# Performance work log

Measured on AMD Instinct MI355X. Metric: run time of the kernel, lower is better.

The kernel has to match this reference:

```python
import jax, jax.numpy as jnp
import numpy as np

B, N, DIN, D, E, STEP = 4, 1024, 256, 256, 5, 5


def setup_inputs() -> dict:
    key = jax.random.key(0)
    ks = jax.random.split(key, 14)
    s = 0.02  # weight init scale
    inp = {
        "node_features": jax.random.normal(ks[0], (B, N, DIN), dtype=jnp.float32),
        # dense per-edge-type adjacency; scaled so messages stay in a sane range
        "adj_matrices": jax.random.uniform(ks[1], (B, E, N, N), dtype=jnp.float32) * (2.0 / N),
        "fc_in_w": jax.random.normal(ks[2], (D, DIN), dtype=jnp.float32) * s,
        "fc_in_b": jnp.zeros((D,), dtype=jnp.float32),
        "edge_w": jax.random.normal(ks[3], (E, D, D), dtype=jnp.float32) * s,
        "edge_b": jax.random.normal(ks[4], (E, D), dtype=jnp.float32) * s,
        "gru_w_ih": jax.random.normal(ks[5], (3 * D, D), dtype=jnp.float32) * s,
        "gru_w_hh": jax.random.normal(ks[6], (3 * D, D), dtype=jnp.float32) * s,
        "gru_b_ih": jnp.zeros((3 * D,), dtype=jnp.float32),
        "gru_b_hh": jnp.zeros((3 * D,), dtype=jnp.float32),
        "conv1_w": jax.random.normal(ks[7], (D, D), dtype=jnp.float32) * s,
        "conv1_b": jnp.zeros((D,), dtype=jnp.float32),
        "conv2_w": jax.random.normal(ks[8], (D, D), dtype=jnp.float32) * s,
        "conv2_b": jnp.zeros((D,), dtype=jnp.float32),
    }
    return inp


def _gru_cell(x, h, w_ih, w_hh, b_ih, b_hh):
    # torch GRUCell: gates ordered [r, z, n]
    gi = x @ w_ih.T + b_ih  # [B*N, 3D]
    gh = h @ w_hh.T + b_hh
    ir, iz, inn = jnp.split(gi, 3, axis=-1)
    hr, hz, hn = jnp.split(gh, 3, axis=-1)
    r = jax.nn.sigmoid(ir + hr)
    z = jax.nn.sigmoid(iz + hz)
    n = jnp.tanh(inn + r * hn)
    return (1.0 - z) * n + z * h


def reference(node_features, adj_matrices, fc_in_w, fc_in_b, edge_w, edge_b,
              gru_w_ih, gru_w_hh, gru_b_ih, gru_b_hh,
              conv1_w, conv1_b, conv2_w, conv2_b):
    h = node_features @ fc_in_w.T + fc_in_b  # [B, N, D]
    sum_edge_b = jnp.sum(edge_b, axis=0)  # accumulated biases over edge types
    for _ in range(STEP):
        # messages per edge type: adj_e @ h  -> [B, E, N, D]
        msgs = jnp.einsum('benm,bmd->bend', adj_matrices, h)
        # per-edge-type linear (y = x @ W_e.T) then accumulate over edge types
        acc = jnp.einsum('bend,ekd->bnk', msgs, edge_w) + sum_edge_b  # [B, N, D]
        h = _gru_cell(acc, h, gru_w_ih, gru_w_hh, gru_b_ih, gru_b_hh)
    node_states = h  # [B, N, D]
    # conv1d with kernel_size=1 over node axis == per-node linear on channels
    attn_weights = jax.nn.sigmoid(node_states @ conv1_w.T + conv1_b)  # [B, N, D]
    feats = jnp.tanh(node_states @ conv2_w.T + conv2_b)  # [B, N, D]
    graph_embedding = jnp.sum(attn_weights * feats, axis=1)  # sum over nodes -> [B, D]
    attn_map = jnp.mean(attn_weights, axis=2)  # mean over channels -> [B, N]
    return (graph_embedding, node_states, attn_map)
```

## Files before the change

kernel.cpp:

```cpp
#include <hip/hip_runtime.h>
#include <hip/hip_bf16.h>
#include <cstdint>


typedef __attribute__((ext_vector_type(8))) short bf16x8;
typedef __attribute__((ext_vector_type(4))) float f32x4;

__device__ __forceinline__ float bf2f(__hip_bfloat16 x) { return __bfloat162float(x); }
__device__ __forceinline__ __hip_bfloat16 f2bf(float x) { return __float2bfloat16(x); }
__device__ __forceinline__ short f2bs(float x) {
  __hip_bfloat16 h = __float2bfloat16(x);
  return *reinterpret_cast<short*>(&h);
}
__device__ __forceinline__ float s2f(short x) {
  __hip_bfloat16 h = *reinterpret_cast<__hip_bfloat16*>(&x);
  return __bfloat162float(h);
}

__device__ __forceinline__ bf16x8 ld8_ext(const void* base, long off, bool f32) {
  if (f32) {
    const float* p = (const float*)base + off;
    bf16x8 r;
#pragma unroll
    for (int i = 0; i < 8; ++i) r[i] = f2bs(p[i]);
    return r;
  }
  return *(const bf16x8*)((const __hip_bfloat16*)base + off);
}

__device__ __forceinline__ bf16x8 ld8_sum5(const __hip_bfloat16* part, int row, int k) {
  const long base = (long)row * 256 + (long)(row >> 10) * 1048576 + k;
  float s[8] = {0.f, 0.f, 0.f, 0.f, 0.f, 0.f, 0.f, 0.f};
#pragma unroll
  for (int e = 0; e < 5; ++e) {
    bf16x8 v = *(const bf16x8*)(part + base + e * 262144);
#pragma unroll
// ... 56 lines not shown
}

__global__ void wcvt_all(const void* fcw, const void* edw, const void* wih,
                         const void* whh, const void* c1w, const void* c2w,
                         const int* __restrict__ flag, __hip_bfloat16* __restrict__ dst) {
  const bool f32 = (*flag != 0);
  const int i = blockIdx.x * 256 + threadIdx.x;
  const void* src; int off;
  if      (i < 65536)  { src = fcw; off = i; }
  else if (i < 393216) { src = edw; off = i - 65536; }
  else if (i < 589824) { src = wih; off = i - 393216; }
  else if (i < 786432) { src = whh; off = i - 589824; }
  else if (i < 851968) { src = c1w; off = i - 786432; }
  else                 { src = c2w; off = i - 851968; }
  dst[i] = f32 ? f2bf(((const float*)src)[off])
               : ((const __hip_bfloat16*)src)[off];
}

__global__ void adj_cvt(const void* __restrict__ src, const int* __restrict__ flag,
                        __hip_bfloat16* __restrict__ dst) {
  const bool f32 = (*flag != 0);
  const long i = ((long)blockIdx.x * 256 + threadIdx.x) * 8;
  bf16x8 r;
  if (f32) {
    const float* p = (const float*)src + i;
#pragma unroll
    for (int j = 0; j < 8; ++j) r[j] = f2bs(p[j]);
  } else {
    r = *(const bf16x8*)((const __hip_bfloat16*)src + i);
  }
  *(bf16x8*)(dst + i) = r;
}

template<bool HAS_BIAS, bool DUAL>
__global__ __launch_bounds__(256)
void gemm_bt128(const __hip_bfloat16* __restrict__ A, const __hip_bfloat16* __restrict__ Bt,
                const float* __restrict__ bias, __hip_bfloat16* __restrict__ C,
                const __hip_bfloat16* __restrict__ A2, const __hip_bfloat16* __restrict__ Bt2,
                const float* __restrict__ bias2, __hip_bfloat16* __restrict__ C2,
                int K, int lda, int ldb, int ldc,
                long aBatch, int zdivA, int zmodA,
                long bBatch, int zdivB, int zmodB,
                long cBatch, int zdivC, int zSplit)
{
  __shared__ __align__(16) __hip_bfloat16 sA[128 * 64];
  __shared__ __align__(16) __hip_bfloat16 sB[64 * 64];
  const int t = threadIdx.x;
  const int w = t >> 6;
  const int l = t & 63;
  const int m0 = blockIdx.x * 128;
  const int n0 = blockIdx.y * 64;
  int z = blockIdx.z;

  const __hip_bfloat16* Au = A; const __hip_bfloat16* Btu = Bt;
  const float* biasu = bias; __hip_bfloat16* Cu = C;
  if (DUAL && z >= zSplit) { Au = A2; Btu = Bt2; biasu = bias2; Cu = C2; z -= zSplit; }

  const __hip_bfloat16* Ab = Au + (long)((z / zdivA) % zmodA) * aBatch;
  const __hip_bfloat16* Bb = Btu + (long)((z / zdivB) % zmodB) * bBatch;

  int sra[4], sca[4];
#pragma unroll
  for (int i = 0; i < 4; ++i) {
    const int p = t + 256 * i;
    sra[i] = p >> 3;
    sca[i] = (p & 7) ^ (sra[i] & 7);
  }
  const int p0 = t, p1 = t + 256;
  const int sr0 = p0 >> 3, sc0 = (p0 & 7) ^ (sr0 & 7);
  const int sr1 = p1 >> 3, sc1 = (p1 & 7) ^ (sr1 & 7);

  f32x4 acc[2][4];
#pragma unroll
  for (int i = 0; i < 2; ++i)
#pragma unroll
    for (int j = 0; j < 4; ++j) acc[i][j] = (f32x4){0.f, 0.f, 0.f, 0.f};

  const int r15 = l & 15;
  const int quad = l >> 4;

  for (int k0 = 0; k0 < K; k0 += 64) {
    bf16x8 av[4];
#pragma unroll
    for (int i = 0; i < 4; ++i)
      av[i] = *(const bf16x8*)(Ab + (long)(m0 + sra[i]) * lda + (k0 + sca[i] * 8));
    bf16x8 b0 = *(const bf16x8*)(Bb + (long)(n0 + sr0) * ldb + (k0 + sc0 * 8));
    bf16x8 b1 = *(const bf16x8*)(Bb + (long)(n0 + sr1) * ldb + (k0 + sc1 * 8));
    __syncthreads();
#pragma unroll
    for (int i = 0; i < 4; ++i) *(bf16x8*)(sA + (t + 256 * i) * 8) = av[i];
    *(bf16x8*)(sB + p0 * 8) = b0;
    *(bf16x8*)(sB + p1 * 8) = b1;
    __syncthreads();
#pragma unroll
    for (int ks = 0; ks < 2; ++ks) {
      const int cg = ks * 4 + quad;
      bf16x8 aF[2], bF[4];
#pragma unroll
      for (int mi = 0; mi < 2; ++mi) {
        const int row = mi * 64 + w * 16 + r15;
        aF[mi] = *(const bf16x8*)(sA + row * 64 + ((cg ^ (row & 7)) * 8));
      }
#pragma unroll
      for (int ni = 0; ni < 4; ++ni) {
        const int nrow = ni * 16 + r15;
        bF[ni] = *(const bf16x8*)(sB + nrow * 64 + ((cg ^ (nrow & 7)) * 8));
      }
#pragma unroll
      for (int mi = 0; mi < 2; ++mi)
#pragma unroll
        for (int ni = 0; ni < 4; ++ni)
          acc[mi][ni] = __builtin_amdgcn_mfma_f32_16x16x32_bf16(
              aF[mi], bF[ni], acc[mi][ni], 0, 0, 0);
    }
  }

  const long cOff = (long)(z / zdivC) * cBatch;
#pragma unroll
  for (int mi = 0; mi < 2; ++mi) {
#pragma unroll
    for (int ni = 0; ni < 4; ++ni) {
      const int n = n0 + ni * 16 + r15;
      float bv = 0.f;
      if (HAS_BIAS) bv = biasu[n];
#pragma unroll
      for (int r = 0; r < 4; ++r) {
        const int m = m0 + mi * 64 + w * 16 + quad * 4 + r;
        Cu[cOff + (long)m * ldc + n] = f2bf(acc[mi][ni][r] + bv);
      }
    }
  }
}

__global__ __launch_bounds__(256)
void part_gh(const __hip_bfloat16* __restrict__ adjb,
             const __hip_bfloat16* __restrict__ heT,
             __hip_bfloat16* __restrict__ part,
             const __hip_bfloat16* __restrict__ hbf,
             const __hip_bfloat16* __restrict__ whh,
             const float* __restrict__ bhh,
             __hip_bfloat16* __restrict__ gh)
{
  __shared__ __align__(16) __hip_bfloat16 sA[128 * 64];
  __shared__ __align__(16) __hip_bfloat16 sB[64 * 64];
  const int t = threadIdx.x;
  const int w = t >> 6;
  const int l = t & 63;
  const int bid = blockIdx.x;

  const __hip_bfloat16* Ab; const __hip_bfloat16* Bb;
  __hip_bfloat16* Cu; const float* biasu = nullptr;
  int K, lda, ldb, ldc, m0, n0;
  bool has_bias;
  if (bid < 640) {
    const int z = bid >> 5, rem = bid & 31;
    m0 = (rem & 7) * 128; n0 = (rem >> 3) * 64;
    Ab = adjb + (long)z * 1048576; lda = 1024; K = 1024;
    Bb = heT + (long)z * 262144;  ldb = 1024;
    Cu = part + (long)z * 262144; ldc = 256;
    has_bias = false;
  } else {
    const int idx = bid - 640;
    m0 = (idx & 31) * 128; n0 = (idx >> 5) * 64;
    Ab = hbf; lda = 256; K = 256;
    Bb = whh; ldb = 256;
    Cu = gh;  ldc = 768;
    biasu = bhh; has_bias = true;
  }

  int sra[4], sca[4];
#pragma unroll
  for (int i = 0; i < 4; ++i) {
    const int p = t + 256 * i;
    sra[i] = p >> 3;
    sca[i] = (p & 7) ^ (sra[i] & 7);
  }
  const int p0 = t, p1 = t + 256;
  const int sr0 = p0 >> 3, sc0 = (p0 & 7) ^ (sr0 & 7);
  const int sr1 = p1 >> 3, sc1 = (p1 & 7) ^ (sr1 & 7);

  f32x4 acc[2][4];
#pragma unroll
  for (int i = 0; i < 2; ++i)
#pragma unroll
    for (int j = 0; j < 4; ++j) acc[i][j] = (f32x4){0.f, 0.f, 0.f, 0.f};

  const int r15 = l & 15;
  const int quad = l >> 4;

  for (int k0 = 0; k0 < K; k0 += 64) {
    bf16x8 av[4];
#pragma unroll
    for (int i = 0; i < 4; ++i)
      av[i] = *(const bf16x8*)(Ab + (long)(m0 + sra[i]) * lda + (k0 + sca[i] * 8));
    bf16x8 b0 = *(const bf16x8*)(Bb + (long)(n0 + sr0) * ldb + (k0 + sc0 * 8));
    bf16x8 b1 = *(const bf16x8*)(Bb + (long)(n0 + sr1) * ldb + (k0 + sc1 * 8));
    __syncthreads();
#pragma unroll
    for (int i = 0; i < 4; ++i) *(bf16x8*)(sA + (t + 256 * i) * 8) = av[i];
    *(bf16x8*)(sB + p0 * 8) = b0;
    *(bf16x8*)(sB + p1 * 8) = b1;
    __syncthreads();
#pragma unroll
    for (int ks = 0; ks < 2; ++ks) {
      const int cg = ks * 4 + quad;
      bf16x8 aF[2], bF[4];
#pragma unroll
      for (int mi = 0; mi < 2; ++mi) {
        const int row = mi * 64 + w * 16 + r15;
        aF[mi] = *(const bf16x8*)(sA + row * 64 + ((cg ^ (row & 7)) * 8));
      }
#pragma unroll
      for (int ni = 0; ni < 4; ++ni) {
        const int nrow = ni * 16 + r15;
        bF[ni] = *(const bf16x8*)(sB + nrow * 64 + ((cg ^ (nrow & 7)) * 8));
      }
#pragma unroll
      for (int mi = 0; mi < 2; ++mi)
#pragma unroll
        for (int ni = 0; ni < 4; ++ni)
          acc[mi][ni] = __builtin_amdgcn_mfma_f32_16x16x32_bf16(
              aF[mi], bF[ni], acc[mi][ni], 0, 0, 0);
    }
  }

#pragma unroll
  for (int mi = 0; mi < 2; ++mi) {
#pragma unroll
    for (int ni = 0; ni < 4; ++ni) {
      const int n = n0 + ni * 16 + r15;
      const float bv = has_bias ? biasu[n] : 0.f;
#pragma unroll
      for (int r = 0; r < 4; ++r) {
        const int m = m0 + mi * 64 + w * 16 + quad * 4 + r;
        Cu[(long)m * ldc + n] = f2bf(acc[mi][ni][r] + bv);
      }
    }
  }
}

__global__ __launch_bounds__(256)
void gi_gate(const __hip_bfloat16* __restrict__ part,
             const __hip_bfloat16* __restrict__ wih,
             const float* __restrict__ biasgi,
             const __hip_bfloat16* __restrict__ gh,
             __hip_bfloat16* __restrict__ hbf,
             void* __restrict__ ns_out, const int* __restrict__ flag)
{
  __shared__ __align__(16) __hip_bfloat16 sA[64 * 64];
  __shared__ __align__(16) __hip_bfloat16 sB0[64 * 64];
  __shared__ __align__(16) __hip_bfloat16 sB1[64 * 64];
  __shared__ __align__(16) __hip_bfloat16 sB2[64 * 64];
  const int t = threadIdx.x;
  const int w = t >> 6;
  const int l = t & 63;
  const int m0 = (blockIdx.x & 63) * 64;
  const int n0 = (blockIdx.x >> 6) * 64;

  const int p0 = t, p1 = t + 256;
  const int sr0 = p0 >> 3, sc0 = (p0 & 7) ^ (sr0 & 7);
  const int sr1 = p1 >> 3, sc1 = (p1 & 7) ^ (sr1 & 7);

  f32x4 acc[3][4];
#pragma unroll
  for (int g = 0; g < 3; ++g)
#pragma unroll
    for (int j = 0; j < 4; ++j) acc[g][j] = (f32x4){0.f, 0.f, 0.f, 0.f};

  const int mrow = w * 16 + (l & 15);
  const int r15 = l & 15;
  const int quad = l >> 4;

  for (int k0 = 0; k0 < 256; k0 += 64) {
    bf16x8 a0 = ld8_sum5(part, m0 + sr0, k0 + sc0 * 8);
    bf16x8 a1 = ld8_sum5(part, m0 + sr1, k0 + sc1 * 8);
    bf16x8 bg[3][2];
#pragma unroll
    for (int g = 0; g < 3; ++g) {
      bg[g][0] = *(const bf16x8*)(wih + (long)(g * 256 + n0 + sr0) * 256 + (k0 + sc0 * 8));
      bg[g][1] = *(const bf16x8*)(wih + (long)(g * 256 + n0 + sr1) * 256 + (k0 + sc1 * 8));
    }
    __syncthreads();
    *(bf16x8*)(sA + p0 * 8) = a0;
    *(bf16x8*)(sA + p1 * 8) = a1;
    *(bf16x8*)(sB0 + p0 * 8) = bg[0][0]; *(bf16x8*)(sB0 + p1 * 8) = bg[0][1];
    *(bf16x8*)(sB1 + p0 * 8) = bg[1][0]; *(bf16x8*)(sB1 + p1 * 8) = bg[1][1];
    *(bf16x8*)(sB2 + p0 * 8) = bg[2][0]; *(bf16x8*)(sB2 + p1 * 8) = bg[2][1];
    __syncthreads();
#pragma unroll
    for (int ks = 0; ks < 2; ++ks) {
      const int cg = ks * 4 + quad;
      bf16x8 af = *(const bf16x8*)(sA + mrow * 64 + ((cg ^ (mrow & 7)) * 8));
#pragma unroll
      for (int t4 = 0; t4 < 4; ++t4) {
        const int nrow = t4 * 16 + r15;
        const int so = nrow * 64 + ((cg ^ (nrow & 7)) * 8);
        bf16x8 b0f = *(const bf16x8*)(sB0 + so);
        bf16x8 b1f = *(const bf16x8*)(sB1 + so);
        bf16x8 b2f = *(const bf16x8*)(sB2 + so);
        acc[0][t4] = __builtin_amdgcn_mfma_f32_16x16x32_bf16(af, b0f, acc[0][t4], 0, 0, 0);
        acc[1][t4] = __builtin_amdgcn_mfma_f32_16x16x32_bf16(af, b1f, acc[1][t4], 0, 0, 0);
        acc[2][t4] = __builtin_amdgcn_mfma_f32_16x16x32_bf16(af, b2f, acc[2][t4], 0, 0, 0);
      }
    }
  }

  const bool f32out = ns_out && (*flag != 0);
#pragma unroll
  for (int t4 = 0; t4 < 4; ++t4) {
    const int n = n0 + t4 * 16 + r15;
    const float bgr = biasgi[n];
    const float bgz = biasgi[256 + n];
    const float bgn = biasgi[512 + n];
#pragma unroll
    for (int r = 0; r < 4; ++r) {
      const int m = m0 + w * 16 + quad * 4 + r;
      const long gb = (long)m * 768;
      const float ir = acc[0][t4][r] + bgr;
      const float iz = acc[1][t4][r] + bgz;
      const float inn = acc[2][t4][r] + bgn;
      const float hr = bf2f(gh[gb + n]);
      const float hz = bf2f(gh[gb + 256 + n]);
      const float hn = bf2f(gh[gb + 512 + n]);
      const long hidx = (long)m * 256 + n;
      const float h = bf2f(hbf[hidx]);
      const float rr = 1.f / (1.f + __expf(-(ir + hr)));
      const float zz = 1.f / (1.f + __expf(-(iz + hz)));
      const float nn = tanhf(inn + rr * hn);
      const float hnew = (1.f - zz) * nn + zz * h;
      const __hip_bfloat16 hb = f2bf(hnew);
      hbf[hidx] = hb;
      if (ns_out) {
        if (f32out) ((float*)ns_out)[1024 + hidx] = hnew;
        else        ((__hip_bfloat16*)ns_out)[1024 + hidx] = hb;
      }
    }
  }
}

template<int OUT_MODE, bool HAS_BIAS, int A_MODE, bool DUAL>
__global__ __launch_bounds__(256)
void gemm_bt(const void* __restrict__ A, const __hip_bfloat16* __restrict__ Bt,
             const float* __restrict__ bias, void* __restrict__ Cp,
             const void* __restrict__ A2, const __hip_bfloat16* __restrict__ Bt2,
             const float* __restrict__ bias2, void* __restrict__ Cp2,
             const int* __restrict__ flag,
             int Kg, int ngrp, int lda, int ldb, int ldc,
             long aBatch, int zdivA, int zmodA,
             long bBatch, int zdivB, int zmodB,
             long cBatch, int zdivC, long aGrp, long bGrp, int zSplit)
{
  __shared__ __align__(16) __hip_bfloat16 sA[64 * 64];
  __shared__ __align__(16) __hip_bfloat16 sB[64 * 64];
  const bool af32 = (A_MODE == 1) ? (*flag != 0) : false;
  const int t = threadIdx.x;
  const int w = t >> 6;
  const int l = t & 63;
  const int m0 = blockIdx.x * 64;
  const int n0 = blockIdx.y * 64;
  int z = blockIdx.z;

  const void* Au = A; const __hip_bfloat16* Btu = Bt;
  const float* biasu = bias; void* Cpu = Cp;
  bool second = false;
  if (DUAL && z >= zSplit) {
    Au = A2; Btu = Bt2; biasu = bias2; Cpu = Cp2; z -= zSplit; second = true;
  }

  const long aOff = (long)((z / zdivA) % zmodA) * aBatch;
  const __hip_bfloat16* Bb = Btu + (long)((z / zdivB) % zmodB) * bBatch;
// ... 81 lines not shown
  bf16x8 vhz = *(const bf16x8*)(gh + gb + 256);
  bf16x8 vhn = *(const bf16x8*)(gh + gb + 512);
  const long hidx = (long)m * 256 + k;
  bf16x8 vh = *(const bf16x8*)(hbf + hidx);
  bf16x8 out;
  float hf[8];
#pragma unroll
  for (int j = 0; j < 8; ++j) {
    const float r = 1.f / (1.f + __expf(-(s2f(vir[j]) + s2f(vhr[j]))));
    const float zz = 1.f / (1.f + __expf(-(s2f(viz[j]) + s2f(vhz[j]))));
    const float nn = tanhf(s2f(vin[j]) + r * s2f(vhn[j]));
    hf[j] = (1.f - zz) * nn + zz * s2f(vh[j]);
    out[j] = f2bs(hf[j]);
  }
  *(bf16x8*)(hbf + hidx) = out;
  if (ns_out) {
    if (*flag) {
      float* o = (float*)ns_out + 1024 + hidx;
#pragma unroll
      for (int j = 0; j < 8; ++j) o[j] = hf[j];
    } else {
      *(bf16x8*)((__hip_bfloat16*)ns_out + 1024 + hidx) = out;
    }
  }
}

__global__ __launch_bounds__(256)
void conv_fused(const __hip_bfloat16* __restrict__ hbf,
                const __hip_bfloat16* __restrict__ c1w,
                const __hip_bfloat16* __restrict__ c2w,
                const float* __restrict__ pool,
                float* __restrict__ geg, float* __restrict__ am32)
{
  __shared__ __align__(16) __hip_bfloat16 sA[64 * 64];
  __shared__ __align__(16) __hip_bfloat16 sB1[64 * 64];
  __shared__ __align__(16) __hip_bfloat16 sB2[64 * 64];
  __shared__ float sge[64];
  __shared__ float sam[64];
  const int t = threadIdx.x, w = t >> 6, l = t & 63;
  const int m0 = blockIdx.x * 64, n0 = blockIdx.y * 64;
  if (t < 64) { sge[t] = 0.f; sam[t] = 0.f; }
  const int p0 = t, p1 = t + 256;
  const int sr0 = p0 >> 3, sc0 = (p0 & 7) ^ (sr0 & 7);
  const int sr1 = p1 >> 3, sc1 = (p1 & 7) ^ (sr1 & 7);
  f32x4 a1[4], a2[4];
#pragma unroll
  for (int i = 0; i < 4; ++i) { a1[i] = (f32x4){0,0,0,0}; a2[i] = (f32x4){0,0,0,0}; }
  const int mrow = w * 16 + (l & 15);
  const int quad = l >> 4;
  for (int k0 = 0; k0 < 256; k0 += 64) {
    bf16x8 va0 = *(const bf16x8*)(hbf + (long)(m0 + sr0) * 256 + (k0 + sc0 * 8));
    bf16x8 va1 = *(const bf16x8*)(hbf + (long)(m0 + sr1) * 256 + (k0 + sc1 * 8));
    bf16x8 vb0 = *(const bf16x8*)(c1w + (long)(n0 + sr0) * 256 + (k0 + sc0 * 8));
    bf16x8 vb1 = *(const bf16x8*)(c1w + (long)(n0 + sr1) * 256 + (k0 + sc1 * 8));
    bf16x8 vc0 = *(const bf16x8*)(c2w + (long)(n0 + sr0) * 256 + (k0 + sc0 * 8));
    bf16x8 vc1 = *(const bf16x8*)(c2w + (long)(n0 + sr1) * 256 + (k0 + sc1 * 8));
    __syncthreads();
    *(bf16x8*)(sA + p0 * 8) = va0;  *(bf16x8*)(sA + p1 * 8) = va1;
    *(bf16x8*)(sB1 + p0 * 8) = vb0; *(bf16x8*)(sB1 + p1 * 8) = vb1;
    *(bf16x8*)(sB2 + p0 * 8) = vc0; *(bf16x8*)(sB2 + p1 * 8) = vc1;
    __syncthreads();
#pragma unroll
    for (int ks = 0; ks < 2; ++ks) {
      const int cg = ks * 4 + quad;
      bf16x8 af = *(const bf16x8*)(sA + mrow * 64 + ((cg ^ (mrow & 7)) * 8));
#pragma unroll
      for (int t4 = 0; t4 < 4; ++t4) {
        const int nrow = t4 * 16 + (l & 15);
        bf16x8 b1f = *(const bf16x8*)(sB1 + nrow * 64 + ((cg ^ (nrow & 7)) * 8));
        bf16x8 b2f = *(const bf16x8*)(sB2 + nrow * 64 + ((cg ^ (nrow & 7)) * 8));
        a1[t4] = __builtin_amdgcn_mfma_f32_16x16x32_bf16(af, b1f, a1[t4], 0, 0, 0);
        a2[t4] = __builtin_amdgcn_mfma_f32_16x16x32_bf16(af, b2f, a2[t4], 0, 0, 0);
      }
    }
  }
  float asum[4] = {0.f, 0.f, 0.f, 0.f};
#pragma unroll
  for (int t4 = 0; t4 < 4; ++t4) {
    const int n = n0 + t4 * 16 + (l & 15);
    const float bb1 = pool[1792 + n], bb2 = pool[2048 + n];
    float g = 0.f;
#pragma unroll
    for (int r = 0; r < 4; ++r) {
      const float av = 1.f / (1.f + __expf(-(a1[t4][r] + bb1)));
      const float fv = tanhf(a2[t4][r] + bb2);
      g += av * fv;
      asum[r] += av;
    }
    atomicAdd(&sge[t4 * 16 + (l & 15)], g);
  }
#pragma unroll
  for (int r = 0; r < 4; ++r) atomicAdd(&sam[w * 16 + quad * 4 + r], asum[r]);
  __syncthreads();
  if (t < 64) atomicAdd(&geg[(m0 >> 10) * 256 + n0 + t], sge[t]);
  else if (t < 128) atomicAdd(&am32[m0 + (t - 64)], sam[t - 64]);
}

__global__ void finish_out(const float* __restrict__ ge, const float* __restrict__ am32,
                           void* __restrict__ dout, const int* __restrict__ flag)
{
  const int t = blockIdx.x * 256 + threadIdx.x;
  const bool f32 = (*flag != 0);
  if (t < 1024) {
    if (f32) ((float*)dout)[t] = ge[t];
    else     ((__hip_bfloat16*)dout)[t] = f2bf(ge[t]);
  } else {
    const float v = am32[t - 1024] * (1.f / 256.f);
    if (f32) ((float*)dout)[1049600 + t - 1024] = v;
    else     ((__hip_bfloat16*)dout)[1049600 + t - 1024] = f2bf(v);
  }
}

extern "C" void kernel_launch(void* const* d_in, const int* in_sizes, int n_in,
                              void* d_out, int out_size, void* d_ws, size_t ws_size,
                              hipStream_t stream) {
  (void)in_sizes; (void)n_in; (void)out_size;
  const void* node_f = d_in[0];
  const void* adj    = d_in[1];
  const void* fc_w   = d_in[2];
  const void* fc_b   = d_in[3];
  const void* edge_w = d_in[4];
  const void* edge_b = d_in[5];
  const void* w_ih   = d_in[6];
  const void* w_hh   = d_in[7];
  const void* b_ih   = d_in[8];
  const void* b_hh   = d_in[9];
  const void* c1w    = d_in[10];
  const void* c1b    = d_in[11];
  const void* c2w    = d_in[12];
  const void* c2b    = d_in[13];

  char* ws = (char*)d_ws;
  const size_t MB = (size_t)1 << 20;
  int*            flag = (int*)(ws);
  float*          bp   = (float*)(ws + 256);
  float*          ge   = (float*)(ws + 14336);
  float*          am32 = (float*)(ws + 18432);
  __hip_bfloat16* wbf  = (__hip_bfloat16*)(ws + 34816);
  __hip_bfloat16* hbf  = (__hip_bfloat16*)(ws + 1869824);
  char*           S    = ws + 3966976;
  __hip_bfloat16* heT  = (__hip_bfloat16*)(S);
  __hip_bfloat16* part = (__hip_bfloat16*)(S + 10 * MB);
  __hip_bfloat16* gi   = (__hip_bfloat16*)(S + 20 * MB);
  __hip_bfloat16* gh   = (__hip_bfloat16*)(S + 26 * MB);
  __hip_bfloat16* adjb = (__hip_bfloat16*)(ws + 40 * MB);

  const bool has_split = ws_size >= 38 * MB;
  const bool has_adjb  = ws_size >= 81 * MB;

  detect_dtype<<<1, 256, 0, stream>>>((const uint32_t*)adj, flag);
  prep_pool<<<1, 256, 0, stream>>>(fc_b, b_ih, b_hh, c1b, c2b, edge_b, flag, bp, ge, am32);
  wcvt_all<<<3584, 256, 0, stream>>>(fc_w, edge_w, w_ih, w_hh, c1w, c2w, flag, wbf);
  bias_gi_k<<<3, 256, 0, stream>>>(bp, wbf + 393216, bp + 2560);
  if (has_adjb) adj_cvt<<<10240, 256, 0, stream>>>(adj, flag, adjb);

  gemm_bt<0, true, 1, false><<<dim3(64, 4, 1), 256, 0, stream>>>(
      node_f, wbf + 0, bp + 0, hbf, nullptr, nullptr, nullptr, nullptr, flag,
      256, 1, 256, 256, 256, 0, 1, 1, 0, 1, 1, 0, 1, 0, 0, 0);

  for (int s = 0; s < 5; ++s) {
    if (has_adjb) {
      gemm_bt128<false, false><<<dim3(2, 16, 20), 256, 0, stream>>>(
          wbf + 65536, hbf, nullptr, heT, nullptr, nullptr, nullptr, nullptr,
          256, 256, 256, 1024,
          65536, 1, 5,
          262144, 5, 4,
          262144, 1, 0);
      part_gh<<<1024, 256, 0, stream>>>(adjb, heT, part,
                                        hbf, wbf + 589824, bp + 1024, gh);
      gi_gate<<<256, 256, 0, stream>>>(part, wbf + 393216, bp + 2560, gh, hbf,
                                       (s == 4) ? d_out : nullptr, flag);
    } else if (has_split) {
      gemm_bt<0, false, 0, false><<<dim3(4, 16, 20), 256, 0, stream>>>(
          wbf + 65536, hbf, nullptr, heT, nullptr, nullptr, nullptr, nullptr, flag,
          256, 1, 256, 256, 1024,
          65536, 1, 5, 262144, 5, 4,
          262144, 1, 0, 0, 0);
      gemm_bt<0, false, 1, false><<<dim3(16, 4, 20), 256, 0, stream>>>(
          adj, heT, nullptr, part, nullptr, nullptr, nullptr, nullptr, flag,
          1024, 1, 1024, 1024, 256,
          1048576, 1, 20, 262144, 1, 20,
          262144, 1, 0, 0, 0);
      gemm_bt<0, true, 2, true><<<dim3(64, 12, 2), 256, 0, stream>>>(
          part, wbf + 393216, bp + 2560, gi,
          hbf,  wbf + 589824, bp + 1024, gh, flag,
          256, 1, 256, 256, 768, 0, 1, 1, 0, 1, 1, 0, 1, 0, 0, 1);
      gru_gate8<<<512, 256, 0, stream>>>(gi, gh, hbf,
                                         (s == 4) ? d_out : nullptr, flag);
    } else {
      gemm_bt<0, false, 0, false><<<dim3(4, 16, 20), 256, 0, stream>>>(
          wbf + 65536, hbf, nullptr, heT, nullptr, nullptr, nullptr, nullptr, flag,
          256, 1, 256, 256, 1024,
          65536, 1, 5, 262144, 5, 4,
          262144, 1, 0, 0, 0);
      gemm_bt<0, true, 1, false><<<dim3(16, 4, 4), 256, 0, stream>>>(
          adj, heT, bp + 2304, part, nullptr, nullptr, nullptr, nullptr, flag,
          1024, 5, 1024, 1024, 256,
          (long)5 * 1048576, 1, 4, (long)5 * 262144, 1, 4,
          262144, 1, 1048576, 262144, 0);
      gemm_bt<0, true, 0, true><<<dim3(64, 12, 2), 256, 0, stream>>>(
          part, wbf + 393216, bp + 256, gi,
          hbf,  wbf + 589824, bp + 1024, gh, flag,
          256, 1, 256, 256, 768, 0, 1, 1, 0, 1, 1, 0, 1, 0, 0, 1);
      gru_gate8<<<512, 256, 0, stream>>>(gi, gh, hbf,
                                         (s == 4) ? d_out : nullptr, flag);
    }
  }

  conv_fused<<<dim3(64, 4), 256, 0, stream>>>(hbf, wbf + 786432, wbf + 851968,
                                              bp, ge, am32);
  finish_out<<<20, 256, 0, stream>>>(ge, am32, d_out, flag);
}
```

Baseline: 432.8 us.

## Fuse GGNN steps into one persistent cooperative kernel with grid syncs

```diff
diff --git a/kernel.cpp b/kernel.cpp
--- a/kernel.cpp
+++ b/kernel.cpp
@@ -1,7 +1,10 @@
 #include <hip/hip_runtime.h>
 #include <hip/hip_bf16.h>
+#include <hip/hip_cooperative_groups.h>
 #include <cstdint>
 
+
+namespace cg = cooperative_groups;
 
 typedef __attribute__((ext_vector_type(8))) short bf16x8;
 typedef __attribute__((ext_vector_type(4))) float f32x4;
@@ -124,33 +127,16 @@
   *(bf16x8*)(dst + i) = r;
 }
 
-template<bool HAS_BIAS, bool DUAL>
-__global__ __launch_bounds__(256)
-void gemm_bt128(const __hip_bfloat16* __restrict__ A, const __hip_bfloat16* __restrict__ Bt,
-                const float* __restrict__ bias, __hip_bfloat16* __restrict__ C,
-                const __hip_bfloat16* __restrict__ A2, const __hip_bfloat16* __restrict__ Bt2,
-                const float* __restrict__ bias2, __hip_bfloat16* __restrict__ C2,
-                int K, int lda, int ldb, int ldc,
-                long aBatch, int zdivA, int zmodA,
-                long bBatch, int zdivB, int zmodB,
-                long cBatch, int zdivC, int zSplit)
-{
-  __shared__ __align__(16) __hip_bfloat16 sA[128 * 64];
-  __shared__ __align__(16) __hip_bfloat16 sB[64 * 64];
-  const int t = threadIdx.x;
-  const int w = t >> 6;
-  const int l = t & 63;
-  const int m0 = blockIdx.x * 128;
-  const int n0 = blockIdx.y * 64;
-  int z = blockIdx.z;
-
-  const __hip_bfloat16* Au = A; const __hip_bfloat16* Btu = Bt;
-  const float* biasu = bias; __hip_bfloat16* Cu = C;
-  if (DUAL && z >= zSplit) { Au = A2; Btu = Bt2; biasu = bias2; Cu = C2; z -= zSplit; }
-
-  const __hip_bfloat16* Ab = Au + (long)((z / zdivA) % zmodA) * aBatch;
-  const __hip_bfloat16* Bb = Btu + (long)((z / zdivB) % zmodB) * bBatch;
-
+
+__device__ __forceinline__ void tile128(char* smem, int t,
+    const void* Abase, int lda, bool af32,
+    const __hip_bfloat16* Bb, int ldb,
+    const float* bias, __hip_bfloat16* C, int ldc,
+    int K, int m0, int n0)
+{
+  __hip_bfloat16* sA = (__hip_bfloat16*)smem;
+  __hip_bfloat16* sB = (__hip_bfloat16*)(smem + 16384);
+  const int w = t >> 6, l = t & 63;
   int sra[4], sca[4];
 #pragma unroll
   for (int i = 0; i < 4; ++i) {
@@ -175,7 +161,7 @@
     bf16x8 av[4];
 #pragma unroll
     for (int i = 0; i < 4; ++i)
-      av[i] = *(const bf16x8*)(Ab + (long)(m0 + sra[i]) * lda + (k0 + sca[i] * 8));
+      av[i] = ld8_ext(Abase, (long)(m0 + sra[i]) * lda + (k0 + sca[i] * 8), af32);
     bf16x8 b0 = *(const bf16x8*)(Bb + (long)(n0 + sr0) * ldb + (k0 + sc0 * 8));
     bf16x8 b1 = *(const bf16x8*)(Bb + (long)(n0 + sr1) * ldb + (k0 + sc1 * 8));
     __syncthreads();
@@ -207,152 +193,36 @@
     }
   }
 
-  const long cOff = (long)(z / zdivC) * cBatch;
+  const bool hasb = (bias != nullptr);
 #pragma unroll
   for (int mi = 0; mi < 2; ++mi) {
 #pragma unroll
     for (int ni = 0; ni < 4; ++ni) {
       const int n = n0 + ni * 16 + r15;
-      float bv = 0.f;
-      if (HAS_BIAS) bv = biasu[n];
+      const float bv = hasb ? bias[n] : 0.f;
 #pragma unroll
       for (int r = 0; r < 4; ++r) {
         const int m = m0 + mi * 64 + w * 16 + quad * 4 + r;
-        Cu[cOff + (long)m * ldc + n] = f2bf(acc[mi][ni][r] + bv);
+        C[(long)m * ldc + n] = f2bf(acc[mi][ni][r] + bv);
       }
     }
   }
 }
 
-__global__ __launch_bounds__(256)
-void part_gh(const __hip_bfloat16* __restrict__ adjb,
-             const __hip_bfloat16* __restrict__ heT,
-             __hip_bfloat16* __restrict__ part,
-             const __hip_bfloat16* __restrict__ hbf,
-             const __hip_bfloat16* __restrict__ whh,
-             const float* __restrict__ bhh,
-             __hip_bfloat16* __restrict__ gh)
-{
-  __shared__ __align__(16) __hip_bfloat16 sA[128 * 64];
-  __shared__ __align__(16) __hip_bfloat16 sB[64 * 64];
-  const int t = threadIdx.x;
-  const int w = t >> 6;
-  const int l = t & 63;
-  const int bid = blockIdx.x;
-
-  const __hip_bfloat16* Ab; const __hip_bfloat16* Bb;
-  __hip_bfloat16* Cu; const float* biasu = nullptr;
-  int K, lda, ldb, ldc, m0, n0;
-  bool has_bias;
-  if (bid < 640) {
-    const int z = bid >> 5, rem = bid & 31;
-    m0 = (rem & 7) * 128; n0 = (rem >> 3) * 64;
-    Ab = adjb + (long)z * 1048576; lda = 1024; K = 1024;
-    Bb = heT + (long)z * 262144;  ldb = 1024;
-    Cu = part + (long)z * 262144; ldc = 256;
-    has_bias = false;
-  } else {
-    const int idx = bid - 640;
-    m0 = (idx & 31) * 128; n0 = (idx >> 5) * 64;
-    Ab = hbf; lda = 256; K = 256;
-    Bb = whh; ldb = 256;
-    Cu = gh;  ldc = 768;
-    biasu = bhh; has_bias = true;
-  }
-
-  int sra[4], sca[4];
-#pragma unroll
-  for (int i = 0; i < 4; ++i) {
-    const int p = t + 256 * i;
-    sra[i] = p >> 3;
-    sca[i] = (p & 7) ^ (sra[i] & 7);
-  }
+__device__ __forceinline__ void gi_tile(char* smem, int t,
+    const __hip_bfloat16* ms, const __hip_bfloat16* wih,
+    const float* biasgi, const __hip_bfloat16* gh,
+    __hip_bfloat16* hbf, void* ns_out, bool f32flag, int m0, int n0)
+{
+  __hip_bfloat16* sA  = (__hip_bfloat16*)smem;
+  __hip_bfloat16* sB0 = (__hip_bfloat16*)(smem + 8192);
+  __hip_bfloat16* sB1 = (__hip_bfloat16*)(smem + 16384);
+  __hip_bfloat16* sB2 = (__hip_bfloat16*)(smem + 24576);
+  const int w = t >> 6, l = t & 63;
   const int p0 = t, p1 = t + 256;
   const int sr0 = p0 >> 3, sc0 = (p0 & 7) ^ (sr0 & 7);
   const int sr1 = p1 >> 3, sc1 = (p1 & 7) ^ (sr1 & 7);
 
-  f32x4 acc[2][4];
-#pragma unroll
-  for (int i = 0; i < 2; ++i)
-#pragma unroll
-    for (int j = 0; j < 4; ++j) acc[i][j] = (f32x4){0.f, 0.f, 0.f, 0.f};
-
-  const int r15 = l & 15;
-  const int quad = l >> 4;
-
-  for (int k0 = 0; k0 < K; k0 += 64) {
-    bf16x8 av[4];
-#pragma unroll
-    for (int i = 0; i < 4; ++i)
-      av[i] = *(const bf16x8*)(Ab + (long)(m0 + sra[i]) * lda + (k0 + sca[i] * 8));
-    bf16x8 b0 = *(const bf16x8*)(Bb + (long)(n0 + sr0) * ldb + (k0 + sc0 * 8));
-    bf16x8 b1 = *(const bf16x8*)(Bb + (long)(n0 + sr1) * ldb + (k0 + sc1 * 8));
-    __syncthreads();
-#pragma unroll
-    for (int i = 0; i < 4; ++i) *(bf16x8*)(sA + (t + 256 * i) * 8) = av[i];
-    *(bf16x8*)(sB + p0 * 8) = b0;
-    *(bf16x8*)(sB + p1 * 8) = b1;
-    __syncthreads();
-#pragma unroll
-    for (int ks = 0; ks < 2; ++ks) {
-      const int cg = ks * 4 + quad;
-      bf16x8 aF[2], bF[4];
-#pragma unroll
-      for (int mi = 0; mi < 2; ++mi) {
-        const int row = mi * 64 + w * 16 + r15;
-        aF[mi] = *(const bf16x8*)(sA + row * 64 + ((cg ^ (row & 7)) * 8));
-      }
-#pragma unroll
-      for (int ni = 0; ni < 4; ++ni) {
-        const int nrow = ni * 16 + r15;
-        bF[ni] = *(const bf16x8*)(sB + nrow * 64 + ((cg ^ (nrow & 7)) * 8));
-      }
-#pragma unroll
-      for (int mi = 0; mi < 2; ++mi)
-#pragma unroll
-        for (int ni = 0; ni < 4; ++ni)
-          acc[mi][ni] = __builtin_amdgcn_mfma_f32_16x16x32_bf16(
-              aF[mi], bF[ni], acc[mi][ni], 0, 0, 0);
-    }
-  }
-
-#pragma unroll
-  for (int mi = 0; mi < 2; ++mi) {
-#pragma unroll
-    for (int ni = 0; ni < 4; ++ni) {
-      const int n = n0 + ni * 16 + r15;
-      const float bv = has_bias ? biasu[n] : 0.f;
-#pragma unroll
-      for (int r = 0; r < 4; ++r) {
-        const int m = m0 + mi * 64 + w * 16 + quad * 4 + r;
-        Cu[(long)m * ldc + n] = f2bf(acc[mi][ni][r] + bv);
-      }
-    }
-  }
-}
-
-__global__ __launch_bounds__(256)
-void gi_gate(const __hip_bfloat16* __restrict__ part,
-             const __hip_bfloat16* __restrict__ wih,
-             const float* __restrict__ biasgi,
-             const __hip_bfloat16* __restrict__ gh,
-             __hip_bfloat16* __restrict__ hbf,
-             void* __restrict__ ns_out, const int* __restrict__ flag)
-{
-  __shared__ __align__(16) __hip_bfloat16 sA[64 * 64];
-  __shared__ __align__(16) __hip_bfloat16 sB0[64 * 64];
-  __shared__ __align__(16) __hip_bfloat16 sB1[64 * 64];
-  __shared__ __align__(16) __hip_bfloat16 sB2[64 * 64];
-  const int t = threadIdx.x;
-  const int w = t >> 6;
-  const int l = t & 63;
-  const int m0 = (blockIdx.x & 63) * 64;
-  const int n0 = (blockIdx.x >> 6) * 64;
-
-  const int p0 = t, p1 = t + 256;
-  const int sr0 = p0 >> 3, sc0 = (p0 & 7) ^ (sr0 & 7);
-  const int sr1 = p1 >> 3, sc1 = (p1 & 7) ^ (sr1 & 7);
-
   f32x4 acc[3][4];
 #pragma unroll
   for (int g = 0; g < 3; ++g)
@@ -364,8 +234,8 @@
   const int quad = l >> 4;
 
   for (int k0 = 0; k0 < 256; k0 += 64) {
-    bf16x8 a0 = ld8_sum5(part, m0 + sr0, k0 + sc0 * 8);
-    bf16x8 a1 = ld8_sum5(part, m0 + sr1, k0 + sc1 * 8);
+    bf16x8 a0 = ld8_sum5(ms, m0 + sr0, k0 + sc0 * 8);
+    bf16x8 a1 = ld8_sum5(ms, m0 + sr1, k0 + sc1 * 8);
     bf16x8 bg[3][2];
 #pragma unroll
     for (int g = 0; g < 3; ++g) {
@@ -397,7 +267,7 @@
     }
   }
 
-  const bool f32out = ns_out && (*flag != 0);
+  const bool f32out = (ns_out != nullptr) && f32flag;
 #pragma unroll
   for (int t4 = 0; t4 < 4; ++t4) {
     const int n = n0 + t4 * 16 + r15;
@@ -428,6 +298,211 @@
       }
     }
   }
+}
+
+__device__ __forceinline__ void conv_tile(char* smem, int t,
+    const __hip_bfloat16* hbf, const __hip_bfloat16* c1w,
+    const __hip_bfloat16* c2w, const float* pool,
+    float* geg, float* am32, int m0, int n0)
+{
+  __hip_bfloat16* sA  = (__hip_bfloat16*)smem;
+  __hip_bfloat16* sB1 = (__hip_bfloat16*)(smem + 8192);
+  __hip_bfloat16* sB2 = (__hip_bfloat16*)(smem + 16384);
+  float* sge = (float*)(smem + 24576);
+  float* sam = (float*)(smem + 24832);
+  const int w = t >> 6, l = t & 63;
+  if (t < 64) { sge[t] = 0.f; sam[t] = 0.f; }
+  const int p0 = t, p1 = t + 256;
+  const int sr0 = p0 >> 3, sc0 = (p0 & 7) ^ (sr0 & 7);
+  const int sr1 = p1 >> 3, sc1 = (p1 & 7) ^ (sr1 & 7);
+  f32x4 a1[4], a2[4];
+#pragma unroll
+  for (int i = 0; i < 4; ++i) { a1[i] = (f32x4){0,0,0,0}; a2[i] = (f32x4){0,0,0,0}; }
+  const int mrow = w * 16 + (l & 15);
+  const int quad = l >> 4;
+  for (int k0 = 0; k0 < 256; k0 += 64) {
+    bf16x8 va0 = *(const bf16x8*)(hbf + (long)(m0 + sr0) * 256 + (k0 + sc0 * 8));
+    bf16x8 va1 = *(const bf16x8*)(hbf + (long)(m0 + sr1) * 256 + (k0 + sc1 * 8));
+    bf16x8 vb0 = *(const bf16x8*)(c1w + (long)(n0 + sr0) * 256 + (k0 + sc0 * 8));
+    bf16x8 vb1 = *(const bf16x8*)(c1w + (long)(n0 + sr1) * 256 + (k0 + sc1 * 8));
+    bf16x8 vc0 = *(const bf16x8*)(c2w + (long)(n0 + sr0) * 256 + (k0 + sc0 * 8));
+    bf16x8 vc1 = *(const bf16x8*)(c2w + (long)(n0 + sr1) * 256 + (k0 + sc1 * 8));
+    __syncthreads();
+    *(bf16x8*)(sA + p0 * 8) = va0;  *(bf16x8*)(sA + p1 * 8) = va1;
+    *(bf16x8*)(sB1 + p0 * 8) = vb0; *(bf16x8*)(sB1 + p1 * 8) = vb1;
+    *(bf16x8*)(sB2 + p0 * 8) = vc0; *(bf16x8*)(sB2 + p1 * 8) = vc1;
+    __syncthreads();
+#pragma unroll
+    for (int ks = 0; ks < 2; ++ks) {
+      const int cg = ks * 4 + quad;
+      bf16x8 af = *(const bf16x8*)(sA + mrow * 64 + ((cg ^ (mrow & 7)) * 8));
+#pragma unroll
+      for (int t4 = 0; t4 < 4; ++t4) {
+        const int nrow = t4 * 16 + (l & 15);
+        bf16x8 b1f = *(const bf16x8*)(sB1 + nrow * 64 + ((cg ^ (nrow & 7)) * 8));
+        bf16x8 b2f = *(const bf16x8*)(sB2 + nrow * 64 + ((cg ^ (nrow & 7)) * 8));
+        a1[t4] = __builtin_amdgcn_mfma_f32_16x16x32_bf16(af, b1f, a1[t4], 0, 0, 0);
+        a2[t4] = __builtin_amdgcn_mfma_f32_16x16x32_bf16(af, b2f, a2[t4], 0, 0, 0);
+      }
+    }
+  }
+  float asum[4] = {0.f, 0.f, 0.f, 0.f};
+#pragma unroll
+  for (int t4 = 0; t4 < 4; ++t4) {
+    const int n = n0 + t4 * 16 + (l & 15);
+    const float bb1 = pool[1792 + n], bb2 = pool[2048 + n];
+    float g = 0.f;
+#pragma unroll
+    for (int r = 0; r < 4; ++r) {
+      const float av = 1.f / (1.f + __expf(-(a1[t4][r] + bb1)));
+      const float fv = tanhf(a2[t4][r] + bb2);
+      g += av * fv;
+      asum[r] += av;
+    }
+    atomicAdd(&sge[t4 * 16 + (l & 15)], g);
+  }
+#pragma unroll
+  for (int r = 0; r < 4; ++r) atomicAdd(&sam[w * 16 + quad * 4 + r], asum[r]);
+  __syncthreads();
+  if (t < 64) atomicAdd(&geg[(m0 >> 10) * 256 + n0 + t], sge[t]);
+  else if (t < 128) atomicAdd(&am32[m0 + (t - 64)], sam[t - 64]);
+}
+
+__global__ __launch_bounds__(256, 2)
+void ggnn_all(const __hip_bfloat16* wbf, const float* bp,
+              const void* node_f, const __hip_bfloat16* adjb,
+              __hip_bfloat16* hbf, __hip_bfloat16* heT,
+              __hip_bfloat16* ms, __hip_bfloat16* gh,
+              float* geg, float* am32, void* dout, const int* flag)
+{
+  cg::grid_group gg = cg::this_grid();
+  __shared__ __align__(16) char smem[32768];
+  const int t = threadIdx.x;
+  const bool f32 = (*flag != 0);
+  const __hip_bfloat16* fcw = wbf;
+  const __hip_bfloat16* ew  = wbf + 65536;
+  const __hip_bfloat16* wih = wbf + 393216;
+  const __hip_bfloat16* whh = wbf + 589824;
+  const __hip_bfloat16* c1w = wbf + 786432;
+  const __hip_bfloat16* c2w = wbf + 851968;
+
+  for (int it = blockIdx.x; it < 128; it += gridDim.x) {
+    const int m0 = (it & 31) * 128, n0 = (it >> 5) * 64;
+    tile128(smem, t, node_f, 256, f32, fcw, 256, bp + 0, hbf, 256, 256, m0, n0);
+  }
+  __threadfence(); gg.sync();
+
+  for (int s = 0; s < 5; ++s) {
+    for (int it = blockIdx.x; it < 640; it += gridDim.x) {
+      const int z = it >> 5, rem = it & 31;
+      const int m0 = (rem & 1) * 128, n0 = (rem >> 1) * 64;
+      tile128(smem, t, ew + (z % 5) * 65536, 256, false,
+              hbf + (long)(z / 5) * 262144, 256,
+              nullptr, heT + (long)z * 262144, 1024, 256, m0, n0);
+    }
+    __threadfence(); gg.sync();
+    for (int it = blockIdx.x; it < 1024; it += gridDim.x) {
+      if (it < 640) {
+        const int z = it >> 5, rem = it & 31;
+        const int m0 = (rem & 7) * 128, n0 = (rem >> 3) * 64;
+        tile128(smem, t, adjb + (long)z * 1048576, 1024, false,
+                heT + (long)z * 262144, 1024,
+                nullptr, ms + (long)z * 262144, 256, 1024, m0, n0);
+      } else {
+        const int idx = it - 640;
+        const int m0 = (idx & 31) * 128, n0 = (idx >> 5) * 64;
+        tile128(smem, t, hbf, 256, false, whh, 256,
+                bp + 1024, gh, 768, 256, m0, n0);
+      }
+    }
+    __threadfence(); gg.sync();
+    void* ns = (s == 4) ? dout : nullptr;
+    for (int it = blockIdx.x; it < 256; it += gridDim.x) {
+      const int m0 = (it & 63) * 64, n0 = (it >> 6) * 64;
+      gi_tile(smem, t, ms, wih, bp + 2560, gh, hbf, ns, f32, m0, n0);
+    }
+    __threadfence(); gg.sync();
+  }
+
+  for (int it = blockIdx.x; it < 256; it += gridDim.x) {
+    const int m0 = (it & 63) * 64, n0 = (it >> 6) * 64;
+    conv_tile(smem, t, hbf, c1w, c2w, bp, geg, am32, m0, n0);
+  }
+  __threadfence(); gg.sync();
+  for (int it = blockIdx.x; it < 20; it += gridDim.x) {
+    const int tt = it * 256 + t;
+    if (tt < 1024) {
+      if (f32) ((float*)dout)[tt] = geg[tt];
+      else     ((__hip_bfloat16*)dout)[tt] = f2bf(geg[tt]);
+    } else {
+      const float v = am32[tt - 1024] * (1.f / 256.f);
+      if (f32) ((float*)dout)[1049600 + tt - 1024] = v;
+      else     ((__hip_bfloat16*)dout)[1049600 + tt - 1024] = f2bf(v);
+    }
+  }
+}
+
+template<bool HAS_BIAS, bool DUAL>
+__global__ __launch_bounds__(256)
+void gemm_bt128(const __hip_bfloat16* __restrict__ A, const __hip_bfloat16* __restrict__ Bt,
+                const float* __restrict__ bias, __hip_bfloat16* __restrict__ C,
+                const __hip_bfloat16* __restrict__ A2, const __hip_bfloat16* __restrict__ Bt2,
+                const float* __restrict__ bias2, __hip_bfloat16* __restrict__ C2,
+                int K, int lda, int ldb, int ldc,
+                long aBatch, int zdivA, int zmodA,
+                long bBatch, int zdivB, int zmodB,
+                long cBatch, int zdivC, int zSplit)
+{
+  __shared__ __align__(16) char smem[24576];
+  const int t = threadIdx.x;
+  const int m0 = blockIdx.x * 128;
+  const int n0 = blockIdx.y * 64;
+  int z = blockIdx.z;
+  const __hip_bfloat16* Au = A; const __hip_bfloat16* Btu = Bt;
+  const float* biasu = bias; __hip_bfloat16* Cu = C;
+  if (DUAL && z >= zSplit) { Au = A2; Btu = Bt2; biasu = bias2; Cu = C2; z -= zSplit; }
+  const __hip_bfloat16* Ab = Au + (long)((z / zdivA) % zmodA) * aBatch;
+  const __hip_bfloat16* Bb = Btu + (long)((z / zdivB) % zmodB) * bBatch;
+  tile128(smem, t, Ab, lda, false, Bb, ldb, HAS_BIAS ? biasu : nullptr,
+          Cu + (long)(z / zdivC) * cBatch, ldc, K, m0, n0);
+}
+
+__global__ __launch_bounds__(256)
+void part_gh(const __hip_bfloat16* __restrict__ adjb,
+             const __hip_bfloat16* __restrict__ heT,
+             __hip_bfloat16* __restrict__ part,
+             const __hip_bfloat16* __restrict__ hbf,
+             const __hip_bfloat16* __restrict__ whh,
+             const float* __restrict__ bhh,
+             __hip_bfloat16* __restrict__ gh)
+{
+  __shared__ __align__(16) char smem[24576];
+  const int t = threadIdx.x;
+  const int bid = blockIdx.x;
+  if (bid < 640) {
+    const int z = bid >> 5, rem = bid & 31;
+    tile128(smem, t, adjb + (long)z * 1048576, 1024, false,
+            heT + (long)z * 262144, 1024, nullptr,
+            part + (long)z * 262144, 256, 1024,
+            (rem & 7) * 128, (rem >> 3) * 64);
+  } else {
+    const int idx = bid - 640;
+    tile128(smem, t, hbf, 256, false, whh, 256, bhh, gh, 768, 256,
+            (idx & 31) * 128, (idx >> 5) * 64);
+  }
+}
+
+__global__ __launch_bounds__(256)
+void gi_gate(const __hip_bfloat16* __restrict__ part,
+             const __hip_bfloat16* __restrict__ wih,
+             const float* __restrict__ biasgi,
+             const __hip_bfloat16* __restrict__ gh,
+             __hip_bfloat16* __restrict__ hbf,
+             void* __restrict__ ns_out, const int* __restrict__ flag)
+{
+  __shared__ __align__(16) char smem[32768];
+  gi_tile(smem, threadIdx.x, part, wih, biasgi, gh, hbf, ns_out,
+          (*flag != 0), (blockIdx.x & 63) * 64, (blockIdx.x >> 6) * 64);
 }
 
 template<int OUT_MODE, bool HAS_BIAS, int A_MODE, bool DUAL>
@@ -575,68 +650,9 @@
                 const float* __restrict__ pool,
                 float* __restrict__ geg, float* __restrict__ am32)
 {
-  __shared__ __align__(16) __hip_bfloat16 sA[64 * 64];
-  __shared__ __align__(16) __hip_bfloat16 sB1[64 * 64];
-  __shared__ __align__(16) __hip_bfloat16 sB2[64 * 64];
-  __shared__ float sge[64];
-  __shared__ float sam[64];
-  const int t = threadIdx.x, w = t >> 6, l = t & 63;
-  const int m0 = blockIdx.x * 64, n0 = blockIdx.y * 64;
-  if (t < 64) { sge[t] = 0.f; sam[t] = 0.f; }
-  const int p0 = t, p1 = t + 256;
-  const int sr0 = p0 >> 3, sc0 = (p0 & 7) ^ (sr0 & 7);
-  const int sr1 = p1 >> 3, sc1 = (p1 & 7) ^ (sr1 & 7);
-  f32x4 a1[4], a2[4];
-#pragma unroll
-  for (int i = 0; i < 4; ++i) { a1[i] = (f32x4){0,0,0,0}; a2[i] = (f32x4){0,0,0,0}; }
-  const int mrow = w * 16 + (l & 15);
-  const int quad = l >> 4;
-  for (int k0 = 0; k0 < 256; k0 += 64) {
-    bf16x8 va0 = *(const bf16x8*)(hbf + (long)(m0 + sr0) * 256 + (k0 + sc0 * 8));
-    bf16x8 va1 = *(const bf16x8*)(hbf + (long)(m0 + sr1) * 256 + (k0 + sc1 * 8));
-    bf16x8 vb0 = *(const bf16x8*)(c1w + (long)(n0 + sr0) * 256 + (k0 + sc0 * 8));
-    bf16x8 vb1 = *(const bf16x8*)(c1w + (long)(n0 + sr1) * 256 + (k0 + sc1 * 8));
-    bf16x8 vc0 = *(const bf16x8*)(c2w + (long)(n0 + sr0) * 256 + (k0 + sc0 * 8));
-    bf16x8 vc1 = *(const bf16x8*)(c2w + (long)(n0 + sr1) * 256 + (k0 + sc1 * 8));
-    __syncthreads();
-    *(bf16x8*)(sA + p0 * 8) = va0;  *(bf16x8*)(sA + p1 * 8) = va1;
-    *(bf16x8*)(sB1 + p0 * 8) = vb0; *(bf16x8*)(sB1 + p1 * 8) = vb1;
-    *(bf16x8*)(sB2 + p0 * 8) = vc0; *(bf16x8*)(sB2 + p1 * 8) = vc1;
-    __syncthreads();
-#pragma unroll
-    for (int ks = 0; ks < 2; ++ks) {
-      const int cg = ks * 4 + quad;
-      bf16x8 af = *(const bf16x8*)(sA + mrow * 64 + ((cg ^ (mrow & 7)) * 8));
-#pragma unroll
-      for (int t4 = 0; t4 < 4; ++t4) {
-        const int nrow = t4 * 16 + (l & 15);
-        bf16x8 b1f = *(const bf16x8*)(sB1 + nrow * 64 + ((cg ^ (nrow & 7)) * 8));
-        bf16x8 b2f = *(const bf16x8*)(sB2 + nrow * 64 + ((cg ^ (nrow & 7)) * 8));
-        a1[t4] = __builtin_amdgcn_mfma_f32_16x16x32_bf16(af, b1f, a1[t4], 0, 0, 0);
-        a2[t4] = __builtin_amdgcn_mfma_f32_16x16x32_bf16(af, b2f, a2[t4], 0, 0, 0);
-      }
-    }
-  }
-  float asum[4] = {0.f, 0.f, 0.f, 0.f};
-#pragma unroll
-  for (int t4 = 0; t4 < 4; ++t4) {
-    const int n = n0 + t4 * 16 + (l & 15);
-    const float bb1 = pool[1792 + n], bb2 = pool[2048 + n];
-    float g = 0.f;
-#pragma unroll
-    for (int r = 0; r < 4; ++r) {
-      const float av = 1.f / (1.f + __expf(-(a1[t4][r] + bb1)));
-      const float fv = tanhf(a2[t4][r] + bb2);
-      g += av * fv;
-      asum[r] += av;
-    }
-    atomicAdd(&sge[t4 * 16 + (l & 15)], g);
-  }
-#pragma unroll
-  for (int r = 0; r < 4; ++r) atomicAdd(&sam[w * 16 + quad * 4 + r], asum[r]);
-  __syncthreads();
-  if (t < 64) atomicAdd(&geg[(m0 >> 10) * 256 + n0 + t], sge[t]);
-  else if (t < 128) atomicAdd(&am32[m0 + (t - 64)], sam[t - 64]);
+  __shared__ __align__(16) char smem[25088];
+  conv_tile(smem, threadIdx.x, hbf, c1w, c2w, pool, geg, am32,
+            blockIdx.x * 64, blockIdx.y * 64);
 }
 
 __global__ void finish_out(const float* __restrict__ ge, const float* __restrict__ am32,
@@ -683,7 +699,7 @@
   __hip_bfloat16* hbf  = (__hip_bfloat16*)(ws + 1869824);
   char*           S    = ws + 3966976;
   __hip_bfloat16* heT  = (__hip_bfloat16*)(S);
-  __hip_bfloat16* part = (__hip_bfloat16*)(S + 10 * MB);
+  __hip_bfloat16* ms   = (__hip_bfloat16*)(S + 10 * MB);
   __hip_bfloat16* gi   = (__hip_bfloat16*)(S + 20 * MB);
   __hip_bfloat16* gh   = (__hip_bfloat16*)(S + 26 * MB);
   __hip_bfloat16* adjb = (__hip_bfloat16*)(ws + 40 * MB);
@@ -695,37 +711,66 @@
   prep_pool<<<1, 256, 0, stream>>>(fc_b, b_ih, b_hh, c1b, c2b, edge_b, flag, bp, ge, am32);
   wcvt_all<<<3584, 256, 0, stream>>>(fc_w, edge_w, w_ih, w_hh, c1w, c2w, flag, wbf);
   bias_gi_k<<<3, 256, 0, stream>>>(bp, wbf + 393216, bp + 2560);
-  if (has_adjb) adj_cvt<<<10240, 256, 0, stream>>>(adj, flag, adjb);
-
-  gemm_bt<0, true, 1, false><<<dim3(64, 4, 1), 256, 0, stream>>>(
-      node_f, wbf + 0, bp + 0, hbf, nullptr, nullptr, nullptr, nullptr, flag,
-      256, 1, 256, 256, 256, 0, 1, 1, 0, 1, 1, 0, 1, 0, 0, 0);
-
-  for (int s = 0; s < 5; ++s) {
-    if (has_adjb) {
+
+  if (has_adjb) {
+    adj_cvt<<<10240, 256, 0, stream>>>(adj, flag, adjb);
+
+    int maxB = 0;
+    hipError_t oe = hipOccupancyMaxActiveBlocksPerMultiprocessor(&maxB, ggnn_all, 256, 0);
+    int grid = 0;
+    if (oe == hipSuccess && maxB > 0) {
+      grid = maxB * 256;
+      if (grid > 1024) grid = 1024;
+    }
+    if (grid >= 256) {
+      void* doutL = d_out;
+      void* args[12] = {
+        (void*)&wbf, (void*)&bp, (void*)&node_f, (void*)&adjb,
+        (void*)&hbf, (void*)&heT, (void*)&ms, (void*)&gh,
+        (void*)&ge, (void*)&am32, (void*)&doutL, (void*)&flag };
+      hipError_t le = hipLaunchCooperativeKernel(
+          (void*)ggnn_all, dim3(grid), dim3(256), args, 0, stream);
+      if (le == hipSuccess) return;
+    }
+
+    gemm_bt<0, true, 1, false><<<dim3(64, 4, 1), 256, 0, stream>>>(
+        node_f, wbf + 0, bp + 0, hbf, nullptr, nullptr, nullptr, nullptr, flag,
+        256, 1, 256, 256, 256, 0, 1, 1, 0, 1, 1, 0, 1, 0, 0, 0);
+    for (int s = 0; s < 5; ++s) {
       gemm_bt128<false, false><<<dim3(2, 16, 20), 256, 0, stream>>>(
           wbf + 65536, hbf, nullptr, heT, nullptr, nullptr, nullptr, nullptr,
           256, 256, 256, 1024,
           65536, 1, 5,
           262144, 5, 4,
           262144, 1, 0);
-      part_gh<<<1024, 256, 0, stream>>>(adjb, heT, part,
+      part_gh<<<1024, 256, 0, stream>>>(adjb, heT, ms,
                                         hbf, wbf + 589824, bp + 1024, gh);
-      gi_gate<<<256, 256, 0, stream>>>(part, wbf + 393216, bp + 2560, gh, hbf,
+      gi_gate<<<256, 256, 0, stream>>>(ms, wbf + 393216, bp + 2560, gh, hbf,
                                        (s == 4) ? d_out : nullptr, flag);
-    } else if (has_split) {
+    }
+    conv_fused<<<dim3(64, 4), 256, 0, stream>>>(hbf, wbf + 786432, wbf + 851968,
+                                                bp, ge, am32);
+    finish_out<<<20, 256, 0, stream>>>(ge, am32, d_out, flag);
+    return;
+  }
+
+  gemm_bt<0, true, 1, false><<<dim3(64, 4, 1), 256, 0, stream>>>(
+      node_f, wbf + 0, bp + 0, hbf, nullptr, nullptr, nullptr, nullptr, flag,
+      256, 1, 256, 256, 256, 0, 1, 1, 0, 1, 1, 0, 1, 0, 0, 0);
+  for (int s = 0; s < 5; ++s) {
+    if (has_split) {
       gemm_bt<0, false, 0, false><<<dim3(4, 16, 20), 256, 0, stream>>>(
           wbf + 65536, hbf, nullptr, heT, nullptr, nullptr, nullptr, nullptr, flag,
           256, 1, 256, 256, 1024,
           65536, 1, 5, 262144, 5, 4,
           262144, 1, 0, 0, 0);
       gemm_bt<0, false, 1, false><<<dim3(16, 4, 20), 256, 0, stream>>>(
-          adj, heT, nullptr, part, nullptr, nullptr, nullptr, nullptr, flag,
+          adj, heT, nullptr, ms, nullptr, nullptr, nullptr, nullptr, flag,
           1024, 1, 1024, 1024, 256,
           1048576, 1, 20, 262144, 1, 20,
           262144, 1, 0, 0, 0);
       gemm_bt<0, true, 2, true><<<dim3(64, 12, 2), 256, 0, stream>>>(
-          part, wbf + 393216, bp + 2560, gi,
+          ms, wbf + 393216, bp + 2560, gi,
           hbf,  wbf + 589824, bp + 1024, gh, flag,
           256, 1, 256, 256, 768, 0, 1, 1, 0, 1, 1, 0, 1, 0, 0, 1);
       gru_gate8<<<512, 256, 0, stream>>>(gi, gh, hbf,
@@ -737,19 +782,18 @@
           65536, 1, 5, 262144, 5, 4,
           262144, 1, 0, 0, 0);
       gemm_bt<0, true, 1, false><<<dim3(16, 4, 4), 256, 0, stream>>>(
-          adj, heT, bp + 2304, part, nullptr, nullptr, nullptr, nullptr, flag,
+          adj, heT, bp + 2304, ms, nullptr, nullptr, nullptr, nullptr, flag,
           1024, 5, 1024, 1024, 256,
           (long)5 * 1048576, 1, 4, (long)5 * 262144, 1, 4,
           262144, 1, 1048576, 262144, 0);
       gemm_bt<0, true, 0, true><<<dim3(64, 12, 2), 256, 0, stream>>>(
-          part, wbf + 393216, bp + 256, gi,
+          ms, wbf + 393216, bp + 256, gi,
           hbf,  wbf + 589824, bp + 1024, gh, flag,
           256, 1, 256, 256, 768, 0, 1, 1, 0, 1, 1, 0, 1, 0, 0, 1);
       gru_gate8<<<512, 256, 0, stream>>>(gi, gh, hbf,
                                          (s == 4) ? d_out : nullptr, flag);
     }
   }
-
   conv_fused<<<dim3(64, 4), 256, 0, stream>>>(hbf, wbf + 786432, wbf + 851968,
                                               bp, ge, am32);
   finish_out<<<20, 256, 0, stream>>>(ge, am32, d_out, flag);
```

After: 1.519 ms. 251% more time.
